# Performance work log

Hardware: AMD Instinct MI355X
Metric: run time of the kernel (lower is better)

Reference implementation:

```python
import jax, jax.numpy as jnp
import numpy as np

N, E = 50000, 400000
C_IN, C_OUT = 64, 32
K = 9  # kernel_size 3x3


def _quad_basis(t):
    # open B-spline basis, degree 2, per torch_spline_conv: k_mod in {0,1,2}
    # t = frac(pseudo * (kernel_size - degree)) = pseudo here (kernel_size=3, degree=2)
    return jnp.stack([0.5 * (1.0 - t) ** 2, -t * t + t + 0.5, 0.5 * t * t], axis=-1)  # [E,3]


def spline_basis(pseudo):
    # kernel_size=[3,3], degree=2, open spline: v = p*(3-2)=p, floor(v)=0 for p in [0,1),
    # so weight index for combination s is exactly s = k_mod0 + 3*k_mod1.
    q0 = _quad_basis(pseudo[:, 0])  # [E,3] varies with s%3
    q1 = _quad_basis(pseudo[:, 1])  # [E,3] varies with s//3
    return (q1[:, :, None] * q0[:, None, :]).reshape(-1, K)  # [E,9]


def spline_conv(x, src, dst, B, W, root, bias, n_nodes):
    xj = x[src]  # gather source node features [E,Cin]
    msg = jnp.zeros((xj.shape[0], W.shape[-1]), x.dtype)
    for k in range(K):  # fixed small kernel loop; avoids [E,K,Cin] blowup
        msg = msg + (xj * B[:, k, None]) @ W[k]
    agg = jax.ops.segment_sum(msg, dst, num_segments=n_nodes)  # aggr='add'
    return agg + x @ root + bias


def setup_inputs() -> dict:
    key = jax.random.key(0)
    ks = jax.random.split(key, 10)
    x = jax.random.normal(ks[0], (N, C_IN), jnp.float32)
    edge_index = jax.random.randint(ks[1], (2, E), 0, N, jnp.int64)
    pseudo = jax.random.uniform(ks[2], (E, 2), jnp.float32)
    skip = jax.random.normal(ks[3], (N, C_OUT), jnp.float32)
    s1 = 1.0 / np.sqrt(C_IN)
    s2 = 1.0 / np.sqrt(C_OUT)
    W1 = jax.random.normal(ks[4], (K, C_IN, C_OUT), jnp.float32) * s1
    root1 = jax.random.normal(ks[5], (C_IN, C_OUT), jnp.float32) * s1
    b1 = jnp.zeros((C_OUT,), jnp.float32)
    W2 = jax.random.normal(ks[6], (K, C_OUT, C_OUT), jnp.float32) * s2
    root2 = jax.random.normal(ks[7], (C_OUT, C_OUT), jnp.float32) * s2
    b2 = jnp.zeros((C_OUT,), jnp.float32)
    return {"x": x, "edge_index": edge_index, "pseudo": pseudo, "skip": skip,
            "W1": W1, "root1": root1, "b1": b1, "W2": W2, "root2": root2, "b2": b2}


def reference(x, edge_index, pseudo, skip, W1, root1, b1, W2, root2, b2):
    src, dst = edge_index[0], edge_index[1]  # flow: source_to_target
    B = spline_basis(pseudo)  # [E,9]
    n = x.shape[0]
    h = jax.nn.relu(spline_conv(x, src, dst, B, W1, root1, b1, n))
    h = jnp.concatenate([h, skip], axis=1)  # [N, Cout+Cskip] == [N, Cin]
    h = jax.nn.relu(spline_conv(h, src, dst, B, W1, root1, b1, n))
    h = jax.nn.relu(spline_conv(h, src, dst, B, W2, root2, b2, n))
    return h
```

## Files before the change

kernel.cpp:

```cpp
#include <hip/hip_runtime.h>
#include <hip/hip_bf16.h>


typedef __attribute__((ext_vector_type(8))) short short8;
typedef __attribute__((ext_vector_type(4))) float f32x4;

__device__ __forceinline__ float blo(unsigned u) {
    union { unsigned u; float f; } x; x.u = u << 16; return x.f;
}
__device__ __forceinline__ float bhi(unsigned u) {
    union { unsigned u; float f; } x; x.u = u & 0xffff0000u; return x.f;
}
__device__ __forceinline__ unsigned short f2bf(float f) {
    union { float f; unsigned u; } x; x.f = f;
    unsigned r = x.u + 0x7fffu + ((x.u >> 16) & 1u);
    return (unsigned short)(r >> 16);
}
__device__ __forceinline__ short8 cvt8(const float* p) {
    float4 a = *(const float4*)p;
    float4 b = *(const float4*)(p + 4);
    short8 r;
    r[0] = (short)f2bf(a.x); r[1] = (short)f2bf(a.y);
    r[2] = (short)f2bf(a.z); r[3] = (short)f2bf(a.w);
    r[4] = (short)f2bf(b.x); r[5] = (short)f2bf(b.y);
    r[6] = (short)f2bf(b.z); r[7] = (short)f2bf(b.w);
    return r;
}

template<int MODE>
__global__ __launch_bounds__(256)
void transform_mfma(const float* __restrict__ Xa, const float* __restrict__ Xb,
                    const unsigned short* __restrict__ Wt,
                    const float* __restrict__ bias,
                    unsigned short* __restrict__ y, float* __restrict__ agg, int N)
{
    const int CIN = (MODE == 2) ? 32 : 64;
    const int t    = threadIdx.x;
    const int wv   = t >> 6;
    const int lane = t & 63;
    const int lc   = lane & 15;
    const int q    = lane >> 4;
    const int base = blockIdx.x * 64 + wv * 16;

    int na = base + lc;
    if (na >= N) na = N - 1;
    short8 a0, a1;
    if (MODE == 0) {
        const float* p = Xa + (size_t)na * 64 + q * 8;
        a0 = cvt8(p);
        a1 = cvt8(p + 32);
    } else if (MODE == 1) {
        a0 = cvt8(Xa + (size_t)na * 32 + q * 8);
        a1 = cvt8(Xb + (size_t)na * 32 + q * 8);
    } else {
        a0 = cvt8(Xa + (size_t)na * 32 + q * 8);
    }

    f32x4 acc[20];
    #pragma unroll
    for (int nt = 0; nt < 20; ++nt) acc[nt] = (f32x4){0.f, 0.f, 0.f, 0.f};

    #pragma unroll
    for (int nt = 0; nt < 20; ++nt) {
        const unsigned short* wp = Wt + ((size_t)(nt * 16 + lc)) * CIN + q * 8;
        acc[nt] = __builtin_amdgcn_mfma_f32_16x16x32_bf16(a0, *(const short8*)wp, acc[nt], 0, 0, 0);
        if (MODE != 2)
            acc[nt] = __builtin_amdgcn_mfma_f32_16x16x32_bf16(a1, *(const short8*)(wp + 32), acc[nt], 0, 0, 0);
    }

    #pragma unroll
    for (int nt = 0; nt < 20; ++nt) {
        #pragma unroll
        for (int r = 0; r < 4; ++r) {
            int n = base + q * 4 + r;
            if (n >= N) continue;
            if (nt < 18) {
                y[(size_t)n * 288 + nt * 16 + lc] = f2bf(acc[nt][r]);
            } else {
                int c = (nt - 18) * 16 + lc;
                agg[(size_t)n * 32 + c] = acc[nt][r] + bias[c];
            }
        }
    }
}

template<int CIN>
__global__ __launch_bounds__(256)
void build_wt_kernel(const float* __restrict__ W, const float* __restrict__ root,
                     unsigned short* __restrict__ Wt)
{
    int idx = blockIdx.x * 256 + threadIdx.x;
    if (idx >= 320 * CIN) return;
    int col = idx / CIN;
    int k   = idx % CIN;
    float v = (col < 288) ? W[((size_t)(col >> 5) * CIN + k) * 32 + (col & 31)]
                          : root[(size_t)k * 32 + (col - 288)];
    Wt[idx] = f2bf(v);
}

__global__ __launch_bounds__(256)
void msg_kernel(const float4* __restrict__ erec,
                const uint4* __restrict__ y4,
                uint4* __restrict__ msg4, int E)
{
    const int t = threadIdx.x;
    const int e = blockIdx.x * 64 + (t >> 2);
    if (e >= E) return;
    const int l = t & 3;

    const float4 r = erec[e];
    const int src = __float_as_int(r.x);
    const int dp  = __float_as_int(r.y);
    const float p0 = r.z, p1 = r.w;

    const float qb[3] = {0.5f * (1.f - p0) * (1.f - p0), -p0 * p0 + p0 + 0.5f, 0.5f * p0 * p0};
    const float qa[3] = {0.5f * (1.f - p1) * (1.f - p1), -p1 * p1 + p1 + 0.5f, 0.5f * p1 * p1};

    const uint4* yb = y4 + (size_t)src * 36 + l;
    float s[8] = {0.f, 0.f, 0.f, 0.f, 0.f, 0.f, 0.f, 0.f};
    #pragma unroll
    for (int a = 0; a < 3; ++a) {
        float z[8] = {0.f, 0.f, 0.f, 0.f, 0.f, 0.f, 0.f, 0.f};
        #pragma unroll
        for (int b = 0; b < 3; ++b) {
            uint4 v = yb[(a * 3 + b) * 4];
            const float cw = qb[b];
            z[0] = fmaf(cw, blo(v.x), z[0]); z[1] = fmaf(cw, bhi(v.x), z[1]);
            z[2] = fmaf(cw, blo(v.y), z[2]); z[3] = fmaf(cw, bhi(v.y), z[3]);
            z[4] = fmaf(cw, blo(v.z), z[4]); z[5] = fmaf(cw, bhi(v.z), z[5]);
            z[6] = fmaf(cw, blo(v.w), z[6]); z[7] = fmaf(cw, bhi(v.w), z[7]);
        }
        #pragma unroll
        for (int j = 0; j < 8; ++j) s[j] = fmaf(qa[a], z[j], s[j]);
    }

    union { uint4 u; __hip_bfloat162 h[4]; } o;
    #pragma unroll
    for (int j = 0; j < 4; ++j)
        o.h[j] = __float22bfloat162_rn(float2{s[2 * j], s[2 * j + 1]});
    msg4[(size_t)dp * 4 + l] = o.u;
}

__global__ __launch_bounds__(256)
void gather_kernel(const int* __restrict__ dstart,
                   const uint4* __restrict__ msg4,
                   float* __restrict__ agg, int N, int E)
{
    const int t = threadIdx.x;
    const int n = blockIdx.x * 64 + (t >> 2);
    if (n >= N) return;
    const int l = t & 3;

    const int e0 = dstart[n] - E;
    const int e1 = ((n + 1 < N) ? dstart[n + 1] : 2 * E) - E;

    float4* ap = (float4*)(agg + (size_t)n * 32 + l * 8);
    float4 A = ap[0], B = ap[1];
    const uint4* mp = msg4 + l;
    for (int e = e0; e < e1; ++e) {
        uint4 v = mp[(size_t)e * 4];
        A.x += blo(v.x); A.y += bhi(v.x); A.z += blo(v.y); A.w += bhi(v.y);
        B.x += blo(v.z); B.y += bhi(v.z); B.z += blo(v.w); B.w += bhi(v.w);
    }
    A.x = fmaxf(A.x, 0.f); A.y = fmaxf(A.y, 0.f); A.z = fmaxf(A.z, 0.f); A.w = fmaxf(A.w, 0.f);
    B.x = fmaxf(B.x, 0.f); B.y = fmaxf(B.y, 0.f); B.z = fmaxf(B.z, 0.f); B.w = fmaxf(B.w, 0.f);
    ap[0] = A; ap[1] = B;
}


__global__ __launch_bounds__(1024)
void zero_kernel(int* __restrict__ p, int n)
{
    int i = blockIdx.x * 1024 + threadIdx.x;
    if (i < n) p[i] = 0;
}

__global__ __launch_bounds__(256)
void count_rank_kernel(const int* __restrict__ ei, int* __restrict__ hist,
                       uint2* __restrict__ rank, int N, int E)
{
    int e = blockIdx.x * 256 + threadIdx.x;
    if (e >= E) return;
    unsigned rs = atomicAdd(&hist[ei[e]], 1);
    unsigned rd = atomicAdd(&hist[N + ei[E + e]], 1);
    rank[e] = uint2{rs, rd};
}

__global__ __launch_bounds__(1024)
void scan1_kernel(int* __restrict__ hist, int* __restrict__ bsum, int n)
{
    __shared__ int s[1024];
    int tid = threadIdx.x;
    int i = blockIdx.x * 1024 + tid;
    int v = (i < n) ? hist[i] : 0;
    s[tid] = v;
    __syncthreads();
    for (int off = 1; off < 1024; off <<= 1) {
        int add = (tid >= off) ? s[tid - off] : 0;
        __syncthreads();
        s[tid] += add;
        __syncthreads();
    }
    if (i < n) hist[i] = s[tid] - v;
    if (tid == 1023) bsum[blockIdx.x] = s[1023];
}

__global__ __launch_bounds__(256)
void scan2_kernel(int* __restrict__ bsum, int nb)
{
    __shared__ int s[256];
    int tid = threadIdx.x;
    int v = (tid < nb) ? bsum[tid] : 0;
    s[tid] = v;
    __syncthreads();
    for (int off = 1; off < 256; off <<= 1) {
        int add = (tid >= off) ? s[tid - off] : 0;
        __syncthreads();
        s[tid] += add;
        __syncthreads();
    }
    if (tid < nb) bsum[tid] = s[tid] - v;
}

__global__ __launch_bounds__(1024)
void scan3_kernel(int* __restrict__ hist, const int* __restrict__ bsum, int n)
{
    int i = blockIdx.x * 1024 + threadIdx.x;
    if (i < n) hist[i] += bsum[blockIdx.x];
}

__global__ __launch_bounds__(256)
void scatter_plain_kernel(const int* __restrict__ ei, const float* __restrict__ pseudo,
                          const int* __restrict__ start, const uint2* __restrict__ rank,
                          float4* __restrict__ erec, int N, int E)
{
    int e = blockIdx.x * 256 + threadIdx.x;
    if (e >= E) return;
    int sv = ei[e];
    int dv = ei[E + e];
    uint2 rk = rank[e];
    int ps = start[sv] + (int)rk.x;
    int pd = start[N + dv] + (int)rk.y - E;
    float4 r;
    r.x = __int_as_float(sv);
    r.y = __int_as_float(pd);
    r.z = pseudo[2 * (size_t)e];
    r.w = pseudo[2 * (size_t)e + 1];
    erec[ps] = r;
}

extern "C" void kernel_launch(void* const* d_in, const int* in_sizes, int n_in,
                              void* d_out, int out_size, void* d_ws, size_t ws_size,
                              hipStream_t stream) {
    const float* x      = (const float*)d_in[0];
    const int*   ei     = (const int*)  d_in[1];
    const float* pseudo = (const float*)d_in[2];
    const float* skip   = (const float*)d_in[3];
    const float* W1     = (const float*)d_in[4];
    const float* root1  = (const float*)d_in[5];
    const float* b1     = (const float*)d_in[6];
    const float* W2     = (const float*)d_in[7];
    const float* root2  = (const float*)d_in[8];
    const float* b2     = (const float*)d_in[9];

    const int N = in_sizes[0] / 64;
    const int E = in_sizes[1] / 2;
    float* out = (float*)d_out;

    unsigned short* y   = (unsigned short*)d_ws;
    unsigned short* msg = y + (size_t)N * 288;
    float*  agg1  = (float*)(msg + (size_t)E * 32);
    float4* erec  = (float4*)(agg1 + (size_t)N * 32);
    uint2*  rank  = (uint2*)(erec + E);
    int*    start = (int*)(rank + E);
    int*    bsum  = start + 2 * N;
    unsigned short* Wt1 = (unsigned short*)(bsum + 256);
    unsigned short* Wt2 = Wt1 + 320 * 64;

    const dim3 blk(256);
    const int tb   = (N + 63) / 64;
    const int eb   = (E + 63) / 64;
    const int gb   = (N + 63) / 64;
    const int e256 = (E + 255) / 256;
    const int n2k  = (2 * N + 1023) / 1024;
    int* dstart = start + N;

    zero_kernel<<<n2k, 1024, 0, stream>>>(start, 2 * N);
    count_rank_kernel<<<e256, blk, 0, stream>>>(ei, start, rank, N, E);
    build_wt_kernel<64><<<(320 * 64 + 255) / 256, blk, 0, stream>>>(W1, root1, Wt1);
    build_wt_kernel<32><<<(320 * 32 + 255) / 256, blk, 0, stream>>>(W2, root2, Wt2);
    scan1_kernel<<<n2k, 1024, 0, stream>>>(start, bsum, 2 * N);
    scan2_kernel<<<1, 256, 0, stream>>>(bsum, n2k);
    scan3_kernel<<<n2k, 1024, 0, stream>>>(start, bsum, 2 * N);
    scatter_plain_kernel<<<e256, blk, 0, stream>>>(ei, pseudo, start, rank, erec, N, E);

    transform_mfma<0><<<tb, blk, 0, stream>>>(x, nullptr, Wt1, b1, y, agg1, N);
    msg_kernel<<<eb, blk, 0, stream>>>(erec, (const uint4*)y, (uint4*)msg, E);
    gather_kernel<<<gb, blk, 0, stream>>>(dstart, (const uint4*)msg, agg1, N, E);
    transform_mfma<1><<<tb, blk, 0, stream>>>(agg1, skip, Wt1, b1, y, agg1, N);
    msg_kernel<<<eb, blk, 0, stream>>>(erec, (const uint4*)y, (uint4*)msg, E);
    gather_kernel<<<gb, blk, 0, stream>>>(dstart, (const uint4*)msg, agg1, N, E);
    transform_mfma<2><<<tb, blk, 0, stream>>>(agg1, nullptr, Wt2, b2, y, out, N);
    msg_kernel<<<eb, blk, 0, stream>>>(erec, (const uint4*)y, (uint4*)msg, E);
    gather_kernel<<<gb, blk, 0, stream>>>(dstart, (const uint4*)msg, out, N, E);
}
```

Before: 278.1 us.

## Fuse per-node transform with edge message computation via shared-memory Y tile

Merges the MFMA node transform and the per-edge message kernel into one kernel. Each block keeps its 64 nodes' 288-wide transformed features in LDS and processes the outgoing edges of those nodes, using the src-sorted CSR start offsets. This removes the global write and random gather of the large per-node y buffer. It also folds weight prep into the histogram zeroing kernel and merges scan2 into scan3, cutting launches. In exchange it uses about 37KB of LDS per block, which lowers occupancy, and the per-block edge loop is uneven across blocks.

```diff
diff --git a/kernel.cpp b/kernel.cpp
--- a/kernel.cpp
+++ b/kernel.cpp
@@ -27,20 +27,27 @@
     return r;
 }
 
+#define YROW 296
+
 template<int MODE>
 __global__ __launch_bounds__(256)
-void transform_mfma(const float* __restrict__ Xa, const float* __restrict__ Xb,
-                    const unsigned short* __restrict__ Wt,
-                    const float* __restrict__ bias,
-                    unsigned short* __restrict__ y, float* __restrict__ agg, int N)
+void layer_tm(const float* __restrict__ Xa, const float* __restrict__ Xb,
+              const unsigned short* __restrict__ Wt,
+              const float* __restrict__ bias,
+              const int* __restrict__ sstart,
+              const float4* __restrict__ erec,
+              float* __restrict__ agg, uint4* __restrict__ msg4, int N, int E)
 {
     const int CIN = (MODE == 2) ? 32 : 64;
+    __shared__ __align__(16) unsigned short sY[64 * YROW];
+
     const int t    = threadIdx.x;
     const int wv   = t >> 6;
     const int lane = t & 63;
     const int lc   = lane & 15;
     const int q    = lane >> 4;
-    const int base = blockIdx.x * 64 + wv * 16;
+    const int n0   = blockIdx.x * 64;
+    const int base = n0 + wv * 16;
 
     int na = base + lc;
     if (na >= N) na = N - 1;
@@ -69,76 +76,61 @@
     }
 
     #pragma unroll
-    for (int nt = 0; nt < 20; ++nt) {
+    for (int nt = 0; nt < 18; ++nt) {
+        #pragma unroll
+        for (int r = 0; r < 4; ++r) {
+            int nl = wv * 16 + q * 4 + r;
+            sY[nl * YROW + nt * 16 + lc] = f2bf(acc[nt][r]);
+        }
+    }
+    #pragma unroll
+    for (int nt = 18; nt < 20; ++nt) {
+        int c = (nt - 18) * 16 + lc;
         #pragma unroll
         for (int r = 0; r < 4; ++r) {
             int n = base + q * 4 + r;
-            if (n >= N) continue;
-            if (nt < 18) {
-                y[(size_t)n * 288 + nt * 16 + lc] = f2bf(acc[nt][r]);
-            } else {
-                int c = (nt - 18) * 16 + lc;
-                agg[(size_t)n * 32 + c] = acc[nt][r] + bias[c];
+            if (n < N) agg[(size_t)n * 32 + c] = acc[nt][r] + bias[c];
+        }
+    }
+    __syncthreads();
+
+    const int e0 = sstart[n0];
+    const int e1 = (n0 + 64 < N) ? sstart[n0 + 64] : E;
+    const int l  = t & 3;
+
+    for (int e = e0 + (t >> 2); e < e1; e += 64) {
+        const float4 r = erec[e];
+        const int srcl = __float_as_int(r.x) - n0;
+        const int dp   = __float_as_int(r.y);
+        const float p0 = r.z, p1 = r.w;
+
+        const float qb[3] = {0.5f * (1.f - p0) * (1.f - p0), -p0 * p0 + p0 + 0.5f, 0.5f * p0 * p0};
+        const float qa[3] = {0.5f * (1.f - p1) * (1.f - p1), -p1 * p1 + p1 + 0.5f, 0.5f * p1 * p1};
+
+        const uint4* yb = (const uint4*)(sY + srcl * YROW) + l;
+        float s[8] = {0.f, 0.f, 0.f, 0.f, 0.f, 0.f, 0.f, 0.f};
+        #pragma unroll
+        for (int a = 0; a < 3; ++a) {
+            float z[8] = {0.f, 0.f, 0.f, 0.f, 0.f, 0.f, 0.f, 0.f};
+            #pragma unroll
+            for (int b = 0; b < 3; ++b) {
+                uint4 v = yb[(a * 3 + b) * 4];
+                const float cw = qb[b];
+                z[0] = fmaf(cw, blo(v.x), z[0]); z[1] = fmaf(cw, bhi(v.x), z[1]);
+                z[2] = fmaf(cw, blo(v.y), z[2]); z[3] = fmaf(cw, bhi(v.y), z[3]);
+                z[4] = fmaf(cw, blo(v.z), z[4]); z[5] = fmaf(cw, bhi(v.z), z[5]);
+                z[6] = fmaf(cw, blo(v.w), z[6]); z[7] = fmaf(cw, bhi(v.w), z[7]);
             }
+            #pragma unroll
+            for (int j = 0; j < 8; ++j) s[j] = fmaf(qa[a], z[j], s[j]);
         }
-    }
-}
-
-template<int CIN>
-__global__ __launch_bounds__(256)
-void build_wt_kernel(const float* __restrict__ W, const float* __restrict__ root,
-                     unsigned short* __restrict__ Wt)
-{
-    int idx = blockIdx.x * 256 + threadIdx.x;
-    if (idx >= 320 * CIN) return;
-    int col = idx / CIN;
-    int k   = idx % CIN;
-    float v = (col < 288) ? W[((size_t)(col >> 5) * CIN + k) * 32 + (col & 31)]
-                          : root[(size_t)k * 32 + (col - 288)];
-    Wt[idx] = f2bf(v);
-}
-
-__global__ __launch_bounds__(256)
-void msg_kernel(const float4* __restrict__ erec,
-                const uint4* __restrict__ y4,
-                uint4* __restrict__ msg4, int E)
-{
-    const int t = threadIdx.x;
-    const int e = blockIdx.x * 64 + (t >> 2);
-    if (e >= E) return;
-    const int l = t & 3;
-
-    const float4 r = erec[e];
-    const int src = __float_as_int(r.x);
-    const int dp  = __float_as_int(r.y);
-    const float p0 = r.z, p1 = r.w;
-
-    const float qb[3] = {0.5f * (1.f - p0) * (1.f - p0), -p0 * p0 + p0 + 0.5f, 0.5f * p0 * p0};
-    const float qa[3] = {0.5f * (1.f - p1) * (1.f - p1), -p1 * p1 + p1 + 0.5f, 0.5f * p1 * p1};
-
-    const uint4* yb = y4 + (size_t)src * 36 + l;
-    float s[8] = {0.f, 0.f, 0.f, 0.f, 0.f, 0.f, 0.f, 0.f};
-    #pragma unroll
-    for (int a = 0; a < 3; ++a) {
-        float z[8] = {0.f, 0.f, 0.f, 0.f, 0.f, 0.f, 0.f, 0.f};
+
+        union { uint4 u; __hip_bfloat162 h[4]; } o;
         #pragma unroll
-        for (int b = 0; b < 3; ++b) {
-            uint4 v = yb[(a * 3 + b) * 4];
-            const float cw = qb[b];
-            z[0] = fmaf(cw, blo(v.x), z[0]); z[1] = fmaf(cw, bhi(v.x), z[1]);
-            z[2] = fmaf(cw, blo(v.y), z[2]); z[3] = fmaf(cw, bhi(v.y), z[3]);
-            z[4] = fmaf(cw, blo(v.z), z[4]); z[5] = fmaf(cw, bhi(v.z), z[5]);
-            z[6] = fmaf(cw, blo(v.w), z[6]); z[7] = fmaf(cw, bhi(v.w), z[7]);
-        }
-        #pragma unroll
-        for (int j = 0; j < 8; ++j) s[j] = fmaf(qa[a], z[j], s[j]);
-    }
-
-    union { uint4 u; __hip_bfloat162 h[4]; } o;
-    #pragma unroll
-    for (int j = 0; j < 4; ++j)
-        o.h[j] = __float22bfloat162_rn(float2{s[2 * j], s[2 * j + 1]});
-    msg4[(size_t)dp * 4 + l] = o.u;
+        for (int j = 0; j < 4; ++j)
+            o.h[j] = __float22bfloat162_rn(float2{s[2 * j], s[2 * j + 1]});
+        msg4[(size_t)dp * 4 + l] = o.u;
+    }
 }
 
 __global__ __launch_bounds__(256)
@@ -168,11 +160,27 @@
 }
 
 
-__global__ __launch_bounds__(1024)
-void zero_kernel(int* __restrict__ p, int n)
-{
-    int i = blockIdx.x * 1024 + threadIdx.x;
-    if (i < n) p[i] = 0;
+__global__ __launch_bounds__(256)
+void init_kernel(int* __restrict__ hist, int n2,
+                 const float* __restrict__ W1, const float* __restrict__ root1,
+                 const float* __restrict__ W2, const float* __restrict__ root2,
+                 unsigned short* __restrict__ Wt1, unsigned short* __restrict__ Wt2)
+{
+    int i = blockIdx.x * 256 + threadIdx.x;
+    if (i < n2) { hist[i] = 0; return; }
+    int j = i - n2;
+    if (j < 320 * 64) {
+        int col = j / 64, k = j % 64;
+        float v = (col < 288) ? W1[((size_t)(col >> 5) * 64 + k) * 32 + (col & 31)]
+                              : root1[(size_t)k * 32 + (col - 288)];
+        Wt1[j] = f2bf(v);
+    } else if (j < 320 * 96) {
+        int jj = j - 320 * 64;
+        int col = jj / 32, k = jj % 32;
+        float v = (col < 288) ? W2[((size_t)(col >> 5) * 32 + k) * 32 + (col & 31)]
+                              : root2[(size_t)k * 32 + (col - 288)];
+        Wt2[jj] = f2bf(v);
+    }
 }
 
 __global__ __launch_bounds__(256)
@@ -205,28 +213,21 @@
     if (tid == 1023) bsum[blockIdx.x] = s[1023];
 }
 
-__global__ __launch_bounds__(256)
-void scan2_kernel(int* __restrict__ bsum, int nb)
-{
-    __shared__ int s[256];
-    int tid = threadIdx.x;
-    int v = (tid < nb) ? bsum[tid] : 0;
-    s[tid] = v;
-    __syncthreads();
-    for (int off = 1; off < 256; off <<= 1) {
-        int add = (tid >= off) ? s[tid - off] : 0;
-        __syncthreads();
-        s[tid] += add;
-        __syncthreads();
-    }
-    if (tid < nb) bsum[tid] = s[tid] - v;
-}
-
 __global__ __launch_bounds__(1024)
 void scan3_kernel(int* __restrict__ hist, const int* __restrict__ bsum, int n)
 {
-    int i = blockIdx.x * 1024 + threadIdx.x;
-    if (i < n) hist[i] += bsum[blockIdx.x];
+    __shared__ int sred[128];
+    int tid = threadIdx.x;
+    int b = blockIdx.x;
+    if (tid < 128) sred[tid] = (tid < b) ? bsum[tid] : 0;
+    __syncthreads();
+    for (int off = 64; off > 0; off >>= 1) {
+        if (tid < off) sred[tid] += sred[tid + off];
+        __syncthreads();
+    }
+    int pre = sred[0];
+    int i = b * 1024 + tid;
+    if (i < n) hist[i] += pre;
 }
 
 __global__ __launch_bounds__(256)
@@ -267,8 +268,7 @@
     const int E = in_sizes[1] / 2;
     float* out = (float*)d_out;
 
-    unsigned short* y   = (unsigned short*)d_ws;
-    unsigned short* msg = y + (size_t)N * 288;
+    unsigned short* msg = (unsigned short*)d_ws;
     float*  agg1  = (float*)(msg + (size_t)E * 32);
     float4* erec  = (float4*)(agg1 + (size_t)N * 32);
     uint2*  rank  = (uint2*)(erec + E);
@@ -279,28 +279,22 @@
 
     const dim3 blk(256);
     const int tb   = (N + 63) / 64;
-    const int eb   = (E + 63) / 64;
     const int gb   = (N + 63) / 64;
     const int e256 = (E + 255) / 256;
     const int n2k  = (2 * N + 1023) / 1024;
+    const int itot = 2 * N + 320 * 96;
     int* dstart = start + N;
 
-    zero_kernel<<<n2k, 1024, 0, stream>>>(start, 2 * N);
+    init_kernel<<<(itot + 255) / 256, blk, 0, stream>>>(start, 2 * N, W1, root1, W2, root2, Wt1, Wt2);
     count_rank_kernel<<<e256, blk, 0, stream>>>(ei, start, rank, N, E);
-    build_wt_kernel<64><<<(320 * 64 + 255) / 256, blk, 0, stream>>>(W1, root1, Wt1);
-    build_wt_kernel<32><<<(320 * 32 + 255) / 256, blk, 0, stream>>>(W2, root2, Wt2);
     scan1_kernel<<<n2k, 1024, 0, stream>>>(start, bsum, 2 * N);
-    scan2_kernel<<<1, 256, 0, stream>>>(bsum, n2k);
     scan3_kernel<<<n2k, 1024, 0, stream>>>(start, bsum, 2 * N);
     scatter_plain_kernel<<<e256, blk, 0, stream>>>(ei, pseudo, start, rank, erec, N, E);
 
-    transform_mfma<0><<<tb, blk, 0, stream>>>(x, nullptr, Wt1, b1, y, agg1, N);
-    msg_kernel<<<eb, blk, 0, stream>>>(erec, (const uint4*)y, (uint4*)msg, E);
+    layer_tm<0><<<tb, blk, 0, stream>>>(x, nullptr, Wt1, b1, start, erec, agg1, (uint4*)msg, N, E);
     gather_kernel<<<gb, blk, 0, stream>>>(dstart, (const uint4*)msg, agg1, N, E);
-    transform_mfma<1><<<tb, blk, 0, stream>>>(agg1, skip, Wt1, b1, y, agg1, N);
-    msg_kernel<<<eb, blk, 0, stream>>>(erec, (const uint4*)y, (uint4*)msg, E);
+    layer_tm<1><<<tb, blk, 0, stream>>>(agg1, skip, Wt1, b1, start, erec, agg1, (uint4*)msg, N, E);
     gather_kernel<<<gb, blk, 0, stream>>>(dstart, (const uint4*)msg, agg1, N, E);
-    transform_mfma<2><<<tb, blk, 0, stream>>>(agg1, nullptr, Wt2, b2, y, out, N);
-    msg_kernel<<<eb, blk, 0, stream>>>(erec, (const uint4*)y, (uint4*)msg, E);
+    layer_tm<2><<<tb, blk, 0, stream>>>(agg1, nullptr, Wt2, b2, start, erec, out, (uint4*)msg, N, E);
     gather_kernel<<<gb, blk, 0, stream>>>(dstart, (const uint4*)msg, out, N, E);
 }
```

After: 265.3 us. 1.05x faster.
